# Kernel tuning notes

Measured on AMD Instinct MI355X. Metric: run time of the kernel, lower is better.

## Reference

```python
import jax, jax.numpy as jnp
import numpy as np

DIM = 1024
HEADS = 16
HEAD_DIM = DIM // HEADS


def _alibi_slopes(n_heads):
    # standard geometric ALiBi slopes
    start = 2.0 ** (-8.0 / n_heads)
    return start ** np.arange(1, n_heads + 1)


def setup_inputs() -> dict:
    key = jax.random.key(0)
    k1, k2, k3 = jax.random.split(key, 3)
    B, T = 2, 2048
    x = jax.random.normal(k1, (B, T, DIM), dtype=jnp.float32)
    # ALiBi bias: slope_h * -(i - j) for j <= i (full matrix here, causal mask applied separately)
    pos = np.arange(T)
    rel = pos[None, :] - pos[:, None]  # (T, T), j - i
    slopes = _alibi_slopes(HEADS)  # (H,)
    alibi_bias = jnp.asarray(slopes[:, None, None] * rel[None, :, :], dtype=jnp.float32)  # (H, T, T)
    # xavier_uniform for weights, zeros for biases
    lim_qkv = float(np.sqrt(6.0 / (DIM + 3 * DIM)))
    Wqkv = jax.random.uniform(k2, (3 * DIM, DIM), minval=-lim_qkv, maxval=lim_qkv, dtype=jnp.float32)
    bqkv = jnp.zeros((3 * DIM,), dtype=jnp.float32)
    lim_out = float(np.sqrt(6.0 / (DIM + DIM)))
    Wout = jax.random.uniform(k3, (DIM, DIM), minval=-lim_out, maxval=lim_out, dtype=jnp.float32)
    bout = jnp.zeros((DIM,), dtype=jnp.float32)
    return {"x": x, "causal": 1, "alibi_bias": alibi_bias,
            "Wqkv": Wqkv, "bqkv": bqkv, "Wout": Wout, "bout": bout}


def reference(x, causal, alibi_bias, Wqkv, bqkv, Wout, bout):
    B, T, D = x.shape
    H, hd = HEADS, HEAD_DIM
    qkv = x @ Wqkv.T + bqkv  # (B, T, 3D)
    q, k, v = jnp.split(qkv, 3, axis=-1)
    def split_heads(t):
        return t.reshape(B, T, H, hd).transpose(0, 2, 1, 3)  # (B, H, T, hd)
    q, k, v = split_heads(q), split_heads(k), split_heads(v)
    scale = 1.0 / jnp.sqrt(jnp.asarray(hd, dtype=q.dtype))
    scores = jnp.einsum('bhqd,bhkd->bhqk', q, k) * scale  # (B, H, T, T)
    bias = alibi_bias[None]  # (1, H, T, T)
    if causal:
        cm = jnp.triu(jnp.ones((T, T), dtype=bool), k=1)
        bias = bias + jnp.where(cm, -jnp.inf, 0.0).astype(q.dtype)
    attn = jax.nn.softmax(scores + bias, axis=-1)
    y = jnp.einsum('bhqk,bhkd->bhqd', attn, v)  # (B, H, T, hd)
    y = y.transpose(0, 2, 1, 3).reshape(B, T, D)
    return y @ Wout.T + bout
```

## Files before the change

### kernel.cpp

```cpp
#include <hip/hip_runtime.h>
#include <cstddef>
#include <cstdint>

#define SEQ    2048
#define DMODEL 1024
#define NH     16
#define HD     64
#define NB     2

typedef __attribute__((ext_vector_type(8))) short short8;
typedef __attribute__((ext_vector_type(4))) float floatx4;

#define MFMA16(a, b, c) __builtin_amdgcn_mfma_f32_16x16x32_bf16((a), (b), (c), 0, 0, 0)

#define ASYNC16(gsrc, ldst) \
    __builtin_amdgcn_global_load_lds((const __attribute__((address_space(1))) void*)(gsrc), \
                                     (__attribute__((address_space(3))) void*)(ldst), 16, 0, 0)

__device__ __forceinline__ short f2bf(float f) {
    union { float f; unsigned u; } a; a.f = f;
    unsigned u = a.u;
    unsigned r = u + 0x7fffu + ((u >> 16) & 1u);
    return (short)(r >> 16);
}

#define NX4 1048576
#define NW4  786432
#define NO4  262144

__global__ __launch_bounds__(256)
void convert_kernel(const float* __restrict__ x, const float* __restrict__ wqkv,
                    const float* __restrict__ wout,
                    short* __restrict__ xb, short* __restrict__ wqkvb,
                    short* __restrict__ woutb)
{
    int i = blockIdx.x * 256 + threadIdx.x;
    const float* src; short* dst; int off;
    if (i < NX4)            { src = x;    dst = xb;    off = i; }
    else if (i < NX4 + NW4) { src = wqkv; dst = wqkvb; off = i - NX4; }
    else if (i < NX4 + NW4 + NO4) { src = wout; dst = woutb; off = i - NX4 - NW4; }
    else return;
    float4 f = ((const float4*)src)[off];
    short4 s;
    s.x = f2bf(f.x); s.y = f2bf(f.y); s.z = f2bf(f.z); s.w = f2bf(f.w);
    ((short4*)dst)[off] = s;
}


__device__ __forceinline__ void gemm_stage(const short* __restrict__ A,
                                           const short* __restrict__ W,
                                           short* As, short* Bs,
                                           int m0, int n0, int k0, int K, int tid)
{
#pragma unroll
    for (int l = 0; l < 4; ++l) {
        int c = l * 256 + tid;
        int row = c >> 3;
        int col8 = (c & 7) ^ (row & 7);
        ASYNC16(&A[(size_t)(m0 + row) * K + k0 + col8 * 8], &As[c * 8]);
        ASYNC16(&W[(size_t)(n0 + row) * K + k0 + col8 * 8], &Bs[c * 8]);
    }
}

__device__ __forceinline__ void gemm_core(const short* As, const short* Bs,
                                          floatx4 acc[4][4], int wm, int wn,
                                          int l15, int quad)
{
#pragma unroll
    for (int kc = 0; kc < 2; ++kc) {
        short8 a[4], b[4];
#pragma unroll
        for (int t = 0; t < 4; ++t) {
            int rowa = wm * 64 + t * 16 + l15;
            int rowb = wn * 64 + t * 16 + l15;
            int sw = (kc * 4 + quad) ^ (l15 & 7);
            a[t] = *(const short8*)&As[(rowa * 8 + sw) * 8];
            b[t] = *(const short8*)&Bs[(rowb * 8 + sw) * 8];
        }
#pragma unroll
        for (int i = 0; i < 4; ++i)
#pragma unroll
            for (int j = 0; j < 4; ++j)
                acc[i][j] = MFMA16(a[i], b[j], acc[i][j]);
    }
}

__global__ __launch_bounds__(256)
void gemm_qkv_bf16(const short* __restrict__ A, const short* __restrict__ W,
                   const float* __restrict__ bias,
                   short* __restrict__ qws, short* __restrict__ kws,
                   short* __restrict__ vtws)
{
    __shared__ short As[128 * 64];
    __shared__ short Bs[128 * 64];
    const int tid = threadIdx.x;
    const int wave = tid >> 6, lane = tid & 63;
    const int l15 = lane & 15, quad = lane >> 4;
    const int wm = wave >> 1, wn = wave & 1;
    const int m0 = blockIdx.y * 128, n0 = blockIdx.x * 128;

    floatx4 acc[4][4];
#pragma unroll
    for (int i = 0; i < 4; ++i)
#pragma unroll
        for (int j = 0; j < 4; ++j) acc[i][j] = (floatx4){0.f, 0.f, 0.f, 0.f};

    for (int k0 = 0; k0 < DMODEL; k0 += 64) {
        __syncthreads();
        gemm_stage(A, W, As, Bs, m0, n0, k0, DMODEL, tid);
        __syncthreads();
        gemm_core(As, Bs, acc, wm, wn, l15, quad);
    }

#pragma unroll
    for (int i = 0; i < 4; ++i) {
#pragma unroll
        for (int j = 0; j < 4; ++j) {
            int n = n0 + wn * 64 + j * 16 + l15;
            int which = n >> 10;
            int rr = n & 1023;
            int h = rr >> 6, d = rr & 63;
            float bv = bias[n];
#pragma unroll
            for (int r = 0; r < 4; ++r) {
                int m = m0 + wm * 64 + i * 16 + quad * 4 + r;
                int bb = m >> 11, t = m & 2047;
                float vv = acc[i][j][r] + bv;
                if (which == 0) vv *= 0.125f;
                short val = f2bf(vv);
                size_t hb = (size_t)(bb * NH + h);
                if (which == 0)      qws[(hb * SEQ + t) * HD + d] = val;
                else if (which == 1) kws[(hb * SEQ + t) * HD + d] = val;
                else                 vtws[(hb * HD + d) * SEQ + t] = val;
            }
        }
    }
}

__global__ __launch_bounds__(256)
void gemm_out_bf16(const short* __restrict__ A, const short* __restrict__ W,
                   const float* __restrict__ bias, float* __restrict__ out)
{
    __shared__ short As[128 * 64];
    __shared__ short Bs[128 * 64];
    const int tid = threadIdx.x;
    const int wave = tid >> 6, lane = tid & 63;
    const int l15 = lane & 15, quad = lane >> 4;
    const int wm = wave >> 1, wn = wave & 1;
    const int m0 = blockIdx.y * 128, n0 = blockIdx.x * 128;

    floatx4 acc[4][4];
#pragma unroll
    for (int i = 0; i < 4; ++i)
#pragma unroll
        for (int j = 0; j < 4; ++j) acc[i][j] = (floatx4){0.f, 0.f, 0.f, 0.f};

    for (int k0 = 0; k0 < DMODEL; k0 += 64) {
        __syncthreads();
        gemm_stage(A, W, As, Bs, m0, n0, k0, DMODEL, tid);
        __syncthreads();
        gemm_core(As, Bs, acc, wm, wn, l15, quad);
    }

#pragma unroll
    for (int i = 0; i < 4; ++i) {
#pragma unroll
        for (int j = 0; j < 4; ++j) {
            int n = n0 + wn * 64 + j * 16 + l15;
            float bv = bias[n];
#pragma unroll
            for (int r = 0; r < 4; ++r) {
                int m = m0 + wm * 64 + i * 16 + quad * 4 + r;
                out[(size_t)m * DMODEL + n] = acc[i][j][r] + bv;
            }
        }
    }
}


#define SCAP 24.0f

__global__ __launch_bounds__(256)
void attn_mfma(const short* __restrict__ q, const short* __restrict__ k,
               const short* __restrict__ vt, const int* __restrict__ causal_p,
               short* __restrict__ y)
{
    const int id = blockIdx.x;
    const int hb = id & 31;
    const int qt = 15 - (id >> 5);
    const int h = hb & 15, b = hb >> 4;

    const int tid = threadIdx.x;
    const int wave = tid >> 6, lane = tid & 63;
    const int l15 = lane & 15, quad = lane >> 4;
    const int q0 = qt * 128;
    const int causal = causal_p[0];
    const float slope = exp2f(-0.5f * (float)(h + 1));

    __shared__ short Ks[64 * 64];
    __shared__ short Vs[64 * 64];

    const size_t base = ((size_t)(b * NH + h)) * SEQ * HD;

    short8 bq[2][2];
    float cc[2];
#pragma unroll
    for (int qt2 = 0; qt2 < 2; ++qt2) {
        int query = q0 + wave * 32 + qt2 * 16 + l15;
        cc[qt2] = SCAP + slope * (float)query;
#pragma unroll
        for (int kc = 0; kc < 2; ++kc)
            bq[qt2][kc] = *(const short8*)&q[base + (size_t)query * HD + kc * 32 + quad * 8];
    }

    float l_acc[2] = {0.f, 0.f};
    floatx4 od[2][4];
#pragma unroll
    for (int qt2 = 0; qt2 < 2; ++qt2)
#pragma unroll
        for (int dt = 0; dt < 4; ++dt) od[qt2][dt] = (floatx4){0.f, 0.f, 0.f, 0.f};

    const int ktmax = causal ? (2 * qt + 1) : (SEQ / 64 - 1);
    for (int kt = 0; kt <= ktmax; ++kt) {
        const int k0 = kt * 64;
        __syncthreads();
#pragma unroll
        for (int l = 0; l < 2; ++l) {
            int c = l * 256 + tid;
            int rho = c >> 3;
            int col8 = (c & 7) ^ (rho & 7);
            int T = rho >> 4, m = rho & 15;
            int kap = (T >> 1) * 32 + (m >> 2) * 8 + (T & 1) * 4 + (m & 3);
            ASYNC16(&k[base + (size_t)(k0 + kap) * HD + col8 * 8], &Ks[c * 8]);
            ASYNC16(&vt[base + (size_t)rho * SEQ + k0 + col8 * 8], &Vs[c * 8]);
        }
        __syncthreads();

        short8 ak[4][2], av[4][2];
#pragma unroll
        for (int T = 0; T < 4; ++T) {
            int row = T * 16 + l15;
#pragma unroll
            for (int kc = 0; kc < 2; ++kc) {
                int sw = (kc * 4 + quad) ^ (row & 7);
                ak[T][kc] = *(const short8*)&Ks[(row * 8 + sw) * 8];
                av[T][kc] = *(const short8*)&Vs[(row * 8 + sw) * 8];
            }
        }

        floatx4 st[2][4];
#pragma unroll
        for (int qt2 = 0; qt2 < 2; ++qt2)
#pragma unroll
            for (int T = 0; T < 4; ++T) {
                floatx4 z = (floatx4){0.f, 0.f, 0.f, 0.f};
                z = MFMA16(ak[T][0], bq[qt2][0], z);
                z = MFMA16(ak[T][1], bq[qt2][1], z);
                st[qt2][T] = z;
            }

        const float kq = slope * (float)(k0 + quad * 8);
#pragma unroll
        for (int qt2 = 0; qt2 < 2; ++qt2) {
            const int qmin = q0 + wave * 32 + qt2 * 16;
            const int query = qmin + l15;
            const bool mrt = causal && (k0 + 63 > qmin);
            float lsum = 0.f;
#pragma unroll
            for (int T = 0; T < 4; ++T) {
                const int koff = (T >> 1) * 32 + (T & 1) * 4;
                const float off = kq + slope * (float)koff - cc[qt2];
#pragma unroll
                for (int r = 0; r < 4; ++r) {
                    float t = st[qt2][T][r] + fmaf(slope, (float)r, off);
                    if (mrt && (k0 + quad * 8 + koff + r > query))
                        t = -__builtin_inff();
                    float p = __expf(t);
                    lsum += p;
                    st[qt2][T][r] = p;
                }
            }
            l_acc[qt2] += lsum;
        }

#pragma unroll
        for (int qt2 = 0; qt2 < 2; ++qt2) {
            union { short8 v; short s[8]; } u0, u1;
#pragma unroll
            for (int j = 0; j < 4; ++j) {
                u0.s[j]     = f2bf(st[qt2][0][j]);
                u0.s[4 + j] = f2bf(st[qt2][1][j]);
                u1.s[j]     = f2bf(st[qt2][2][j]);
                u1.s[4 + j] = f2bf(st[qt2][3][j]);
            }
#pragma unroll
            for (int dt = 0; dt < 4; ++dt) {
                floatx4 oo = od[qt2][dt];
                oo = MFMA16(av[dt][0], u0.v, oo);
                oo = MFMA16(av[dt][1], u1.v, oo);
                od[qt2][dt] = oo;
            }
        }
    }

#pragma unroll
    for (int qt2 = 0; qt2 < 2; ++qt2) {
        l_acc[qt2] += __shfl_xor(l_acc[qt2], 16, 64);
        l_acc[qt2] += __shfl_xor(l_acc[qt2], 32, 64);
    }

#pragma unroll
    for (int qt2 = 0; qt2 < 2; ++qt2) {
        const float inv_l = 1.0f / l_acc[qt2];
        const int row = q0 + wave * 32 + qt2 * 16 + l15;
#pragma unroll
        for (int dt = 0; dt < 4; ++dt) {
            short4 sv;
            sv.x = f2bf(od[qt2][dt][0] * inv_l);
            sv.y = f2bf(od[qt2][dt][1] * inv_l);
            sv.z = f2bf(od[qt2][dt][2] * inv_l);
            sv.w = f2bf(od[qt2][dt][3] * inv_l);
            *(short4*)&y[(size_t)(b * SEQ + row) * DMODEL + h * HD + dt * 16 + quad * 4] = sv;
        }
    }
}


extern "C" void kernel_launch(void* const* d_in, const int* in_sizes, int n_in,
                              void* d_out, int out_size, void* d_ws, size_t ws_size,
                              hipStream_t stream)
{
    const float* x    = (const float*)d_in[0];
    const int*   caus = (const int*)d_in[1];
    const float* Wqkv = (const float*)d_in[3];
    const float* bqkv = (const float*)d_in[4];
    const float* Wout = (const float*)d_in[5];
    const float* bout = (const float*)d_in[6];
    float* out = (float*)d_out;

    char* ws = (char*)d_ws;
    short* xb    = (short*)(ws);
    short* wqkvb = (short*)(ws + (8u  << 20));
    short* woutb = (short*)(ws + (14u << 20));
    short* qws   = (short*)(ws + (16u << 20));
    short* kws   = (short*)(ws + (24u << 20));
    short* vtws  = (short*)(ws + (32u << 20));
    short* yb    = (short*)(ws + (40u << 20));

    convert_kernel<<<8192, 256, 0, stream>>>(x, Wqkv, Wout, xb, wqkvb, woutb);

    dim3 g1(3072 / 128, 4096 / 128);
    gemm_qkv_bf16<<<g1, 256, 0, stream>>>(xb, wqkvb, bqkv, qws, kws, vtws);

    attn_mfma<<<512, 256, 0, stream>>>(qws, kws, vtws, caus, yb);

    dim3 g2(DMODEL / 128, 4096 / 128);
    gemm_out_bf16<<<g2, 256, 0, stream>>>(yb, woutb, bout, out);
}
```

Baseline: 455.7 us.

## Double-buffer attention K/V tiles and retile output GEMM to 128x64 blocks

The attention kernel now keeps two LDS buffers for K and V and issues the async loads for the next key tile before computing on the current one. This overlaps global-to-LDS transfer with the MFMA and softmax work and drops one barrier per iteration. Separately, the output projection GEMM changes from 128x128 to 128x64 tiles, with each wave owning 32 rows, which doubles the block count to fill more CUs. The cost is twice the LDS in attention and more total A-tile reloads in the GEMM.

```diff
diff --git a/kernel.cpp b/kernel.cpp
--- a/kernel.cpp
+++ b/kernel.cpp
@@ -142,35 +142,66 @@
                    const float* __restrict__ bias, float* __restrict__ out)
 {
     __shared__ short As[128 * 64];
-    __shared__ short Bs[128 * 64];
+    __shared__ short Bs[64 * 64];
     const int tid = threadIdx.x;
     const int wave = tid >> 6, lane = tid & 63;
     const int l15 = lane & 15, quad = lane >> 4;
-    const int wm = wave >> 1, wn = wave & 1;
-    const int m0 = blockIdx.y * 128, n0 = blockIdx.x * 128;
-
-    floatx4 acc[4][4];
-#pragma unroll
-    for (int i = 0; i < 4; ++i)
+    const int m0 = blockIdx.y * 128, n0 = blockIdx.x * 64;
+
+    floatx4 acc[2][4];
+#pragma unroll
+    for (int i = 0; i < 2; ++i)
 #pragma unroll
         for (int j = 0; j < 4; ++j) acc[i][j] = (floatx4){0.f, 0.f, 0.f, 0.f};
 
     for (int k0 = 0; k0 < DMODEL; k0 += 64) {
         __syncthreads();
-        gemm_stage(A, W, As, Bs, m0, n0, k0, DMODEL, tid);
+#pragma unroll
+        for (int l = 0; l < 4; ++l) {
+            int c = l * 256 + tid;
+            int row = c >> 3;
+            int col8 = (c & 7) ^ (row & 7);
+            ASYNC16(&A[(size_t)(m0 + row) * DMODEL + k0 + col8 * 8], &As[c * 8]);
+        }
+#pragma unroll
+        for (int l = 0; l < 2; ++l) {
+            int c = l * 256 + tid;
+            int row = c >> 3;
+            int col8 = (c & 7) ^ (row & 7);
+            ASYNC16(&W[(size_t)(n0 + row) * DMODEL + k0 + col8 * 8], &Bs[c * 8]);
+        }
         __syncthreads();
-        gemm_core(As, Bs, acc, wm, wn, l15, quad);
-    }
-
-#pragma unroll
-    for (int i = 0; i < 4; ++i) {
+#pragma unroll
+        for (int kc = 0; kc < 2; ++kc) {
+            int sw = (kc * 4 + quad) ^ (l15 & 7);
+            short8 a[2], b[4];
+#pragma unroll
+            for (int i = 0; i < 2; ++i) {
+                int rowa = wave * 32 + i * 16 + l15;
+                a[i] = *(const short8*)&As[(rowa * 8 + sw) * 8];
+            }
+#pragma unroll
+            for (int j = 0; j < 4; ++j) {
+                int rowb = j * 16 + l15;
+                b[j] = *(const short8*)&Bs[(rowb * 8 + sw) * 8];
+            }
+#pragma unroll
+            for (int i = 0; i < 2; ++i)
+#pragma unroll
+                for (int j = 0; j < 4; ++j)
+                    acc[i][j] = MFMA16(a[i], b[j], acc[i][j]);
+        }
+    }
+
+#pragma unroll
+    for (int i = 0; i < 2; ++i) {
 #pragma unroll
         for (int j = 0; j < 4; ++j) {
-            int n = n0 + wn * 64 + j * 16 + l15;
+            int n = n0 + j * 16 + l15;
             float bv = bias[n];
 #pragma unroll
             for (int r = 0; r < 4; ++r) {
-                int m = m0 + wm * 64 + i * 16 + quad * 4 + r;
+                int m = m0 + wave * 32 + i * 16 + quad * 4 + r;
                 out[(size_t)m * DMODEL + n] = acc[i][j][r] + bv;
             }
         }
@@ -197,8 +228,8 @@
     const int causal = causal_p[0];
     const float slope = exp2f(-0.5f * (float)(h + 1));
 
-    __shared__ short Ks[64 * 64];
-    __shared__ short Vs[64 * 64];
+    __shared__ short Ks[2][64 * 64];
+    __shared__ short Vs[2][64 * 64];
 
     const size_t base = ((size_t)(b * NH + h)) * SEQ * HD;
 
@@ -220,10 +251,10 @@
 #pragma unroll
         for (int dt = 0; dt < 4; ++dt) od[qt2][dt] = (floatx4){0.f, 0.f, 0.f, 0.f};
 
-    const int ktmax = causal ? (2 * qt + 1) : (SEQ / 64 - 1);
-    for (int kt = 0; kt <= ktmax; ++kt) {
-        const int k0 = kt * 64;
-        __syncthreads();
+    auto stage = [&](int kt) {
+        const int k0s = kt * 64;
+        short* Kd = &Ks[kt & 1][0];
+        short* Vd = &Vs[kt & 1][0];
 #pragma unroll
         for (int l = 0; l < 2; ++l) {
             int c = l * 256 + tid;
@@ -231,10 +262,20 @@
             int col8 = (c & 7) ^ (rho & 7);
             int T = rho >> 4, m = rho & 15;
             int kap = (T >> 1) * 32 + (m >> 2) * 8 + (T & 1) * 4 + (m & 3);
-            ASYNC16(&k[base + (size_t)(k0 + kap) * HD + col8 * 8], &Ks[c * 8]);
-            ASYNC16(&vt[base + (size_t)rho * SEQ + k0 + col8 * 8], &Vs[c * 8]);
-        }
+            ASYNC16(&k[base + (size_t)(k0s + kap) * HD + col8 * 8], &Kd[c * 8]);
+            ASYNC16(&vt[base + (size_t)rho * SEQ + k0s + col8 * 8], &Vd[c * 8]);
+        }
+    };
+
+    const int ktmax = causal ? (2 * qt + 1) : (SEQ / 64 - 1);
+    stage(0);
+    for (int kt = 0; kt <= ktmax; ++kt) {
+        const int k0 = kt * 64;
         __syncthreads();
+        if (kt < ktmax) stage(kt + 1);
+
+        const short* Kc = &Ks[kt & 1][0];
+        const short* Vc = &Vs[kt & 1][0];
 
         short8 ak[4][2], av[4][2];
 #pragma unroll
@@ -243,8 +284,8 @@
 #pragma unroll
             for (int kc = 0; kc < 2; ++kc) {
                 int sw = (kc * 4 + quad) ^ (row & 7);
-                ak[T][kc] = *(const short8*)&Ks[(row * 8 + sw) * 8];
-                av[T][kc] = *(const short8*)&Vs[(row * 8 + sw) * 8];
+                ak[T][kc] = *(const short8*)&Kc[(row * 8 + sw) * 8];
+                av[T][kc] = *(const short8*)&Vc[(row * 8 + sw) * 8];
             }
         }
 
@@ -354,6 +395,6 @@
 
     attn_mfma<<<512, 256, 0, stream>>>(qws, kws, vtws, caus, yb);
 
-    dim3 g2(DMODEL / 128, 4096 / 128);
+    dim3 g2(DMODEL / 64, 4096 / 128);
     gemm_out_bf16<<<g2, 256, 0, stream>>>(yb, woutb, bout, out);
 }
```

Measured after the change: 450.5 us. Within noise of the previous version (-1.2%).
